# Optimization experiments

Measured on AMD Instinct MI355X. Metric: run time of the kernel, lower is better.

Reference implementation:

```python
import jax, jax.numpy as jnp
import numpy as np

B, N, D = 2, 2048, 1024
H, WS = 16, 128  # num_heads, window_size
DH = D // H
HALF = WS // 2  # window is [i-HALF, i+HALF] inclusive -> 129 keys interior


def setup_inputs() -> dict:
    key = jax.random.key(0)
    ks = jax.random.split(key, 5)
    return {
        "x": jax.random.normal(ks[0], (B, N, D), dtype=jnp.float32),
        "Wqkv": jax.random.normal(ks[1], (D, 3 * D), dtype=jnp.float32) * 0.02,
        "bqkv": jax.random.normal(ks[2], (3 * D,), dtype=jnp.float32) * 0.02,
        "Wout": jax.random.normal(ks[3], (D, D), dtype=jnp.float32) * 0.02,
        "bout": jax.random.normal(ks[4], (D,), dtype=jnp.float32) * 0.02,
    }


def reference(x, Wqkv, bqkv, Wout, bout):
    b, n, d = x.shape
    scale = DH ** -0.5
    qkv = x @ Wqkv + bqkv  # [b, n, 3d]
    q, k, v = jnp.split(qkv, 3, axis=-1)
    # [b, n, d] -> [b, h, n, dh]
    def heads(t):
        return t.reshape(b, n, H, DH).transpose(0, 2, 1, 3)
    q, k, v = heads(q), heads(k), heads(v)
    scores = jnp.einsum("bhid,bhjd->bhij", q, k) * scale  # [b, h, n, n]
    # per-token window [max(0,i-HALF), min(n,i+HALF+1)) == |i-j| <= HALF
    idx = jnp.arange(n)
    band = jnp.abs(idx[:, None] - idx[None, :]) <= HALF  # [n, n]
    neg = jnp.asarray(jnp.finfo(scores.dtype).min, scores.dtype)
    scores = jnp.where(band[None, None], scores, neg)
    attn = jax.nn.softmax(scores, axis=-1)
    out = jnp.einsum("bhij,bhjd->bhid", attn, v)  # [b, h, n, dh]
    out = out.transpose(0, 2, 1, 3).reshape(b, n, d)
    return out @ Wout + bout
```

## Files before the change

### kernel.cpp

```cpp
#include <hip/hip_runtime.h>
#include <hip/hip_bf16.h>
#include <cstdint>
#include <cstddef>

#define BB 2
#define NN 2048
#define DD 1024
#define HH 16
#define DHH 64
#define SCALE 0.125f

typedef _Float16 f16x8 __attribute__((ext_vector_type(8)));
typedef _Float16 f16x4 __attribute__((ext_vector_type(4)));
typedef float f32x4 __attribute__((ext_vector_type(4)));

#define AS1(p) ((__attribute__((address_space(1))) void*)(p))
#define AS3(p) ((__attribute__((address_space(3))) void*)(p))

__global__ __launch_bounds__(256) void prep(const float* __restrict__ x, _Float16* __restrict__ x_h,
                                            const float* __restrict__ Wqkv, _Float16* __restrict__ Wqkv_t,
                                            const float* __restrict__ Wout, _Float16* __restrict__ Wout_t) {
    __shared__ float tile[32][33];
    int bx = blockIdx.x, tid = threadIdx.x;
    if (bx < 2048) {
        int i = bx * 2048 + tid * 8;
        f32x4 a = *(const f32x4*)(x + i);
        f32x4 b = *(const f32x4*)(x + i + 4);
        f16x8 o;
        o[0] = (_Float16)a[0]; o[1] = (_Float16)a[1]; o[2] = (_Float16)a[2]; o[3] = (_Float16)a[3];
        o[4] = (_Float16)b[0]; o[5] = (_Float16)b[1]; o[6] = (_Float16)b[2]; o[7] = (_Float16)b[3];
        *(f16x8*)(x_h + i) = o;
        return;
    }
    const float* in; _Float16* out; int C, tc, tr;
    if (bx < 5120) { int t = bx - 2048; C = 3 * DD; in = Wqkv; out = Wqkv_t; tc = t % 96; tr = t / 96; }
    else           { int t = bx - 5120; C = DD;     in = Wout; out = Wout_t; tc = t % 32; tr = t / 32; }
    int R = DD;
    int txx = tid & 31, ty = tid >> 5;
    int r0 = tr * 32, c0 = tc * 32;
#pragma unroll
    for (int i = 0; i < 32; i += 8)
        tile[ty + i][txx] = in[(size_t)(r0 + ty + i) * C + (c0 + txx)];
    __syncthreads();
#pragma unroll
    for (int i = 0; i < 32; i += 8)
        out[(size_t)(c0 + ty + i) * R + (r0 + txx)] = (_Float16)tile[txx][ty + i];
}

template <bool SWAP, int MT>
__device__ __forceinline__ void gemm_kloop(const _Float16* __restrict__ gA,
                                           const _Float16* __restrict__ gB,
                                           _Float16* lA, _Float16* lB,
                                           const _Float16* As, const _Float16* Bs,
                                           int wm, int wn, int llo, int lhi, int K,
                                           f32x4 acc[][MT > 4 ? MT : 4]) {
    for (int k0 = 0; k0 < K; k0 += 64) {
        __syncthreads();
#pragma unroll
        for (int p = 0; p < MT; ++p)
            __builtin_amdgcn_global_load_lds(AS1(gA + (size_t)p * 8 * K + k0), AS3(lA + p * 512), 16, 0, 0);
#pragma unroll
        for (int p = 0; p < 4; ++p)
            __builtin_amdgcn_global_load_lds(AS1(gB + (size_t)p * 8 * K + k0), AS3(lB + p * 512), 16, 0, 0);
        __syncthreads();

#pragma unroll
        for (int ks = 0; ks < 2; ++ks) {
            f16x8 af[MT], bf[4];
            int swz = (((ks * 4 + lhi) ^ (llo & 7)) * 8);
#pragma unroll
            for (int mt = 0; mt < MT; ++mt)
                af[mt] = *(const f16x8*)(As + (wm + mt * 16 + llo) * 64 + swz);
#pragma unroll
            for (int nt = 0; nt < 4; ++nt)
                bf[nt] = *(const f16x8*)(Bs + (wn + nt * 16 + llo) * 64 + swz);
            if (SWAP) {
#pragma unroll
                for (int nt = 0; nt < 4; ++nt)
#pragma unroll
                    for (int mt = 0; mt < MT; ++mt)
                        acc[nt][mt] = __builtin_amdgcn_mfma_f32_16x16x32_f16(bf[nt], af[mt], acc[nt][mt], 0, 0, 0);
            } else {
#pragma unroll
                for (int mt = 0; mt < MT; ++mt)
#pragma unroll
                    for (int nt = 0; nt < 4; ++nt)
                        acc[mt][nt] = __builtin_amdgcn_mfma_f32_16x16x32_f16(af[mt], bf[nt], acc[mt][nt], 0, 0, 0);
            }
        }
    }
}

__global__ __launch_bounds__(256) void gemm_qkv(const _Float16* __restrict__ A,
                                                const _Float16* __restrict__ Bt,
                                                const float* __restrict__ bias,
                                                _Float16* __restrict__ q_h,
                                                _Float16* __restrict__ k_h,
                                                _Float16* __restrict__ vt_h) {
    const int K = DD;
    __shared__ __align__(16) _Float16 As[128 * 64];
    __shared__ __align__(16) _Float16 Bs[128 * 64];
    int id = blockIdx.x;
    int xcd = id & 7, j = id >> 3;
    int bn = (xcd * 3 + j % 3) * 128;
    int bm = (j / 3) * 128;
    int tid = threadIdx.x;
    int wave = tid >> 6, lane = tid & 63;
    int wm = (wave >> 1) * 64, wn = (wave & 1) * 64;
    int lhi = lane >> 4, llo = lane & 15;

    f32x4 acc[4][4] = {};

    int srow = wave * 32 + (lane >> 3);
    int scol = ((lane & 7) ^ (lane >> 3)) * 8;
    const _Float16* gA = A + (size_t)(bm + srow) * K + scol;
    const _Float16* gB = Bt + (size_t)(bn + srow) * K + scol;
    _Float16* lA = As + wave * 2048 + lane * 8;
    _Float16* lB = Bs + wave * 2048 + lane * 8;

    int region = bn >> 10;
    if (region == 2) {
        gemm_kloop<false, 4>(gA, gB, lA, lB, As, Bs, wm, wn, llo, lhi, K, acc);
#pragma unroll
        for (int nt = 0; nt < 4; ++nt) {
            int col = bn + wn + nt * 16 + llo;
            float bv = bias[col];
            int c = col & 1023;
            int h = c >> 6, dh = c & 63;
#pragma unroll
            for (int mt = 0; mt < 4; ++mt) {
                int row = bm + wm + mt * 16 + lhi * 4;
                int b = row >> 11, n = row & 2047;
                f16x4 v4;
#pragma unroll
                for (int r = 0; r < 4; ++r) v4[r] = (_Float16)(acc[mt][nt][r] + bv);
                *(f16x4*)(vt_h + ((size_t)((b * HH + h) * DHH + dh)) * NN + n) = v4;
            }
        }
    } else {
        gemm_kloop<true, 4>(gA, gB, lA, lB, As, Bs, wm, wn, llo, lhi, K, acc);
        _Float16* dst0 = (region == 0 ? q_h : k_h);
#pragma unroll
        for (int nt = 0; nt < 4; ++nt) {
            int cbase = bn + wn + nt * 16 + lhi * 4;
            f32x4 b4 = *(const f32x4*)(bias + cbase);
            int c = cbase & 1023;
#pragma unroll
            for (int mt = 0; mt < 4; ++mt) {
                int t = bm + wm + mt * 16 + llo;
                int b = t >> 11, n = t & 2047;
                f16x4 v4;
#pragma unroll
                for (int r = 0; r < 4; ++r) v4[r] = (_Float16)(acc[nt][mt][r] + b4[r]);
                *(f16x4*)(dst0 + (size_t)(b * NN + n) * DD + c) = v4;
            }
        }
    }
}

__global__ __launch_bounds__(256) void gemm_out(const _Float16* __restrict__ A,
                                                const _Float16* __restrict__ Bt,
                                                const float* __restrict__ bias,
                                                float* __restrict__ Cf) {
    const int K = DD, N = DD;
    __shared__ __align__(16) _Float16 As[64 * 64];
    __shared__ __align__(16) _Float16 Bs[128 * 64];
    int id = blockIdx.x;
    int xcd = id & 7, j = id >> 3;
    int bm = (xcd * 8 + (j >> 3)) * 64;
    int bn = (j & 7) * 128;
    int tid = threadIdx.x;
    int wave = tid >> 6, lane = tid & 63;
    int wm = (wave >> 1) * 32, wn = (wave & 1) * 64;
    int lhi = lane >> 4, llo = lane & 15;

    f32x4 acc[4][4] = {};

    int srowA = wave * 16 + (lane >> 3);
    int srowB = wave * 32 + (lane >> 3);
    int scol = ((lane & 7) ^ (lane >> 3)) * 8;
    const _Float16* gA = A + (size_t)(bm + srowA) * K + scol;
    const _Float16* gB = Bt + (size_t)(bn + srowB) * K + scol;
    _Float16* lA = As + wave * 1024 + lane * 8;
    _Float16* lB = Bs + wave * 2048 + lane * 8;

    gemm_kloop<true, 2>(gA, gB, lA, lB, As, Bs, wm, wn, llo, lhi, K,
                        (f32x4(*)[4])acc);

#pragma unroll
    for (int nt = 0; nt < 4; ++nt) {
        int cbase = bn + wn + nt * 16 + lhi * 4;
        f32x4 b4 = *(const f32x4*)(bias + cbase);
#pragma unroll
        for (int mt = 0; mt < 2; ++mt) {
            int t = bm + wm + mt * 16 + llo;
            f32x4 v4;
#pragma unroll
            for (int r = 0; r < 4; ++r) v4[r] = acc[nt][mt][r] + b4[r];
            *(f32x4*)(Cf + (size_t)t * N + cbase) = v4;
        }
    }
}

#define KP 64
#define PP 200
#define VP 200
__global__ __launch_bounds__(256) void local_attn(const _Float16* __restrict__ q_h,
                                                  const _Float16* __restrict__ k_h,
                                                  const _Float16* __restrict__ vt_h,
                                                  _Float16* __restrict__ outh) {
    __shared__ __align__(16) _Float16 Ks[192 * KP];
    __shared__ __align__(16) _Float16 Ps[64 * PP];
    __shared__ __align__(16) _Float16 Vt[64 * VP];
    int tid = threadIdx.x;
    int id = blockIdx.x;
    int xcd = id & 7, j = id >> 3;
    int i0 = (xcd * 4 + (j & 3)) * 64;
    int hb = j >> 2;
    int h = hb & 15, b = hb >> 4;

    int wave = tid >> 6, lane = tid & 63;
    int llo = lane & 15, lhi = lane >> 4;

    {
        int srow = lane >> 3;
        int chunk = ((lane & 7) ^ (lane >> 3)) * 8;
        const _Float16* kb = k_h + (size_t)(b * NN) * DD + h * DHH + chunk;
#pragma unroll
        for (int q = 0; q < 6; ++q) {
            int p = wave * 6 + q;
            int jj = i0 - 64 + p * 8 + srow;
            __builtin_amdgcn_global_load_lds(AS1(kb + (ptrdiff_t)jj * DD), AS3(Ks + p * 512 + lane * 8), 16, 0, 0);
        }
    }

    {
        const _Float16* vb = vt_h + (size_t)((b * HH + h) * DHH) * NN + (i0 - 64);
        for (int u = tid; u < 1536; u += 256) {
            int d = u / 24, c = u % 24;
            f16x8 vv = *(const f16x8*)(vb + (ptrdiff_t)d * NN + c * 8);
            *(f16x8*)(Vt + d * VP + c * 8) = vv;
        }
    }

    int qrow = wave * 16 + llo;
    int qi = i0 + qrow;
    const _Float16* qp = q_h + (size_t)(b * NN + qi) * DD + h * DHH;
    f16x8 qf0 = *(const f16x8*)(qp + lhi * 8);
    f16x8 qf1 = *(const f16x8*)(qp + 32 + lhi * 8);
    __syncthreads();

    float sc[12][4];
#pragma unroll
    for (int mt = 0; mt < 12; ++mt) {
        const _Float16* kr = Ks + (mt * 16 + llo) * 64;
        f16x8 kf0 = *(const f16x8*)(kr + ((lhi ^ (llo & 7)) * 8));
        f16x8 kf1 = *(const f16x8*)(kr + (((lhi + 4) ^ (llo & 7)) * 8));
        f32x4 a = {0.f, 0.f, 0.f, 0.f};
        a = __builtin_amdgcn_mfma_f32_16x16x32_f16(kf0, qf0, a, 0, 0, 0);
        a = __builtin_amdgcn_mfma_f32_16x16x32_f16(kf1, qf1, a, 0, 0, 0);
#pragma unroll
        for (int r = 0; r < 4; ++r) sc[mt][r] = a[r];
    }

    float m = -1e30f;
#pragma unroll
    for (int mt = 0; mt < 12; ++mt)
#pragma unroll
        for (int r = 0; r < 4; ++r) {
            int sidx = mt * 16 + lhi * 4 + r;
            int jj = i0 - 64 + sidx;
            int dj = jj - qi;
            bool valid = (jj >= 0) && (jj < NN) && (dj <= 64) && (dj >= -64);
            float v = valid ? sc[mt][r] * SCALE : -1e30f;
            sc[mt][r] = v;
            m = fmaxf(m, v);
        }
    m = fmaxf(m, __shfl_xor(m, 16, 64));
    m = fmaxf(m, __shfl_xor(m, 32, 64));
    float l = 0.f;
#pragma unroll
    for (int mt = 0; mt < 12; ++mt)
#pragma unroll
        for (int r = 0; r < 4; ++r) {
            float e = __expf(sc[mt][r] - m);
            sc[mt][r] = e;
            l += e;
        }
    l += __shfl_xor(l, 16, 64);
    l += __shfl_xor(l, 32, 64);
    float invl = 1.f / l;

#pragma unroll
    for (int mt = 0; mt < 12; ++mt) {
        f16x4 pv;
#pragma unroll
        for (int r = 0; r < 4; ++r) pv[r] = (_Float16)(sc[mt][r] * invl);
        *(f16x4*)(Ps + qrow * PP + mt * 16 + lhi * 4) = pv;
    }
    __asm__ volatile("s_waitcnt lgkmcnt(0)" ::: "memory");

    f32x4 oacc[4] = {};
#pragma unroll
    for (int ks = 0; ks < 6; ++ks) {
        f16x8 pf = *(const f16x8*)(Ps + (wave * 16 + llo) * PP + ks * 32 + lhi * 8);
#pragma unroll
        for (int nt = 0; nt < 4; ++nt) {
            f16x8 vf = *(const f16x8*)(Vt + (nt * 16 + llo) * VP + ks * 32 + lhi * 8);
            oacc[nt] = __builtin_amdgcn_mfma_f32_16x16x32_f16(pf, vf, oacc[nt], 0, 0, 0);
        }
    }

    _Float16* orow = outh + (size_t)(b * NN) * DD + h * DHH;
#pragma unroll
    for (int nt = 0; nt < 4; ++nt)
#pragma unroll
        for (int r = 0; r < 4; ++r) {
            int q = wave * 16 + lhi * 4 + r;
            int d = nt * 16 + llo;
            orow[(size_t)(i0 + q) * DD + d] = (_Float16)oacc[nt][r];
        }
}

extern "C" void kernel_launch(void* const* d_in, const int* in_sizes, int n_in,
                              void* d_out, int out_size, void* d_ws, size_t ws_size,
                              hipStream_t stream) {
    const float* x    = (const float*)d_in[0];
    const float* Wqkv = (const float*)d_in[1];
    const float* bqkv = (const float*)d_in[2];
    const float* Wout = (const float*)d_in[3];
    const float* bout = (const float*)d_in[4];
    float* out = (float*)d_out;

    char* ws = (char*)d_ws;
    _Float16* x_h    = (_Float16*)(ws);
    _Float16* Wqkv_t = (_Float16*)(ws + (size_t)8  * 1024 * 1024);
    _Float16* Wout_t = (_Float16*)(ws + (size_t)14 * 1024 * 1024);
    _Float16* q_h    = (_Float16*)(ws + (size_t)16 * 1024 * 1024);
    _Float16* k_h    = (_Float16*)(ws + (size_t)24 * 1024 * 1024);
    _Float16* vt_h   = (_Float16*)(ws + (size_t)32 * 1024 * 1024);
    _Float16* attn_h = (_Float16*)(ws + (size_t)40 * 1024 * 1024);

    prep<<<6144, 256, 0, stream>>>(x, x_h, Wqkv, Wqkv_t, Wout, Wout_t);

    gemm_qkv<<<768, 256, 0, stream>>>(x_h, Wqkv_t, bqkv, q_h, k_h, vt_h);

    local_attn<<<1024, 256, 0, stream>>>(q_h, k_h, vt_h, attn_h);

    gemm_out<<<512, 256, 0, stream>>>(attn_h, Wout_t, bout, out);
}
```

Measured before the change: 156.8 us.

## Double-buffer LDS tiles in GEMM k-loops to overlap global loads with MFMA

```diff
diff --git a/kernel.cpp b/kernel.cpp
--- a/kernel.cpp
+++ b/kernel.cpp
@@ -48,32 +48,52 @@
 }
 
 template <bool SWAP, int MT>
-__device__ __forceinline__ void gemm_kloop(const _Float16* __restrict__ gA,
-                                           const _Float16* __restrict__ gB,
-                                           _Float16* lA, _Float16* lB,
-                                           const _Float16* As, const _Float16* Bs,
-                                           int wm, int wn, int llo, int lhi, int K,
-                                           f32x4 acc[][MT > 4 ? MT : 4]) {
-    for (int k0 = 0; k0 < K; k0 += 64) {
-        __syncthreads();
-#pragma unroll
-        for (int p = 0; p < MT; ++p)
-            __builtin_amdgcn_global_load_lds(AS1(gA + (size_t)p * 8 * K + k0), AS3(lA + p * 512), 16, 0, 0);
-#pragma unroll
-        for (int p = 0; p < 4; ++p)
-            __builtin_amdgcn_global_load_lds(AS1(gB + (size_t)p * 8 * K + k0), AS3(lB + p * 512), 16, 0, 0);
-        __syncthreads();
-
+__device__ __forceinline__ void gemm_kloop_pipe(const _Float16* __restrict__ gA,
+                                                const _Float16* __restrict__ gB,
+                                                _Float16* lA0, _Float16* lB0,
+                                                _Float16* lA1, _Float16* lB1,
+                                                const _Float16* As0, const _Float16* Bs0,
+                                                const _Float16* As1, const _Float16* Bs1,
+                                                int wm, int wn, int llo, int lhi, int K,
+                                                f32x4 acc[][MT > 4 ? MT : 4]) {
+    const int NIT = K / 64;
+#pragma unroll
+    for (int p = 0; p < MT; ++p)
+        __builtin_amdgcn_global_load_lds(AS1(gA + (size_t)p * 8 * K), AS3(lA0 + p * 512), 16, 0, 0);
+#pragma unroll
+    for (int p = 0; p < 4; ++p)
+        __builtin_amdgcn_global_load_lds(AS1(gB + (size_t)p * 8 * K), AS3(lB0 + p * 512), 16, 0, 0);
+
+    for (int it = 0; it < NIT; ++it) {
+        if (it + 1 < NIT) {
+            int k1 = (it + 1) * 64;
+            _Float16* nlA = (it & 1) ? lA0 : lA1;
+            _Float16* nlB = (it & 1) ? lB0 : lB1;
+#pragma unroll
+            for (int p = 0; p < MT; ++p)
+                __builtin_amdgcn_global_load_lds(AS1(gA + (size_t)p * 8 * K + k1), AS3(nlA + p * 512), 16, 0, 0);
+#pragma unroll
+            for (int p = 0; p < 4; ++p)
+                __builtin_amdgcn_global_load_lds(AS1(gB + (size_t)p * 8 * K + k1), AS3(nlB + p * 512), 16, 0, 0);
+            if (MT == 4) asm volatile("s_waitcnt vmcnt(8)" ::: "memory");
+            else         asm volatile("s_waitcnt vmcnt(6)" ::: "memory");
+        } else {
+            asm volatile("s_waitcnt vmcnt(0)" ::: "memory");
+        }
+        asm volatile("s_barrier" ::: "memory");
+
+        const _Float16* cAs = (it & 1) ? As1 : As0;
+        const _Float16* cBs = (it & 1) ? Bs1 : Bs0;
 #pragma unroll
         for (int ks = 0; ks < 2; ++ks) {
             f16x8 af[MT], bf[4];
             int swz = (((ks * 4 + lhi) ^ (llo & 7)) * 8);
 #pragma unroll
             for (int mt = 0; mt < MT; ++mt)
-                af[mt] = *(const f16x8*)(As + (wm + mt * 16 + llo) * 64 + swz);
+                af[mt] = *(const f16x8*)(cAs + (wm + mt * 16 + llo) * 64 + swz);
 #pragma unroll
             for (int nt = 0; nt < 4; ++nt)
-                bf[nt] = *(const f16x8*)(Bs + (wn + nt * 16 + llo) * 64 + swz);
+                bf[nt] = *(const f16x8*)(cBs + (wn + nt * 16 + llo) * 64 + swz);
             if (SWAP) {
 #pragma unroll
                 for (int nt = 0; nt < 4; ++nt)
@@ -88,6 +108,8 @@
                         acc[mt][nt] = __builtin_amdgcn_mfma_f32_16x16x32_f16(af[mt], bf[nt], acc[mt][nt], 0, 0, 0);
             }
         }
+        asm volatile("s_waitcnt lgkmcnt(0)" ::: "memory");
+        asm volatile("s_barrier" ::: "memory");
     }
 }
 
@@ -98,8 +120,8 @@
                                                 _Float16* __restrict__ k_h,
                                                 _Float16* __restrict__ vt_h) {
     const int K = DD;
-    __shared__ __align__(16) _Float16 As[128 * 64];
-    __shared__ __align__(16) _Float16 Bs[128 * 64];
+    __shared__ __align__(16) _Float16 As0[128 * 64], As1[128 * 64];
+    __shared__ __align__(16) _Float16 Bs0[128 * 64], Bs1[128 * 64];
     int id = blockIdx.x;
     int xcd = id & 7, j = id >> 3;
     int bn = (xcd * 3 + j % 3) * 128;
@@ -115,12 +137,12 @@
     int scol = ((lane & 7) ^ (lane >> 3)) * 8;
     const _Float16* gA = A + (size_t)(bm + srow) * K + scol;
     const _Float16* gB = Bt + (size_t)(bn + srow) * K + scol;
-    _Float16* lA = As + wave * 2048 + lane * 8;
-    _Float16* lB = Bs + wave * 2048 + lane * 8;
+    int loff = wave * 2048 + lane * 8;
 
     int region = bn >> 10;
     if (region == 2) {
-        gemm_kloop<false, 4>(gA, gB, lA, lB, As, Bs, wm, wn, llo, lhi, K, acc);
+        gemm_kloop_pipe<false, 4>(gA, gB, As0 + loff, Bs0 + loff, As1 + loff, Bs1 + loff,
+                                  As0, Bs0, As1, Bs1, wm, wn, llo, lhi, K, acc);
 #pragma unroll
         for (int nt = 0; nt < 4; ++nt) {
             int col = bn + wn + nt * 16 + llo;
@@ -138,7 +160,8 @@
             }
         }
     } else {
-        gemm_kloop<true, 4>(gA, gB, lA, lB, As, Bs, wm, wn, llo, lhi, K, acc);
+        gemm_kloop_pipe<true, 4>(gA, gB, As0 + loff, Bs0 + loff, As1 + loff, Bs1 + loff,
+                                 As0, Bs0, As1, Bs1, wm, wn, llo, lhi, K, acc);
         _Float16* dst0 = (region == 0 ? q_h : k_h);
 #pragma unroll
         for (int nt = 0; nt < 4; ++nt) {
@@ -163,8 +186,8 @@
                                                 const float* __restrict__ bias,
                                                 float* __restrict__ Cf) {
     const int K = DD, N = DD;
-    __shared__ __align__(16) _Float16 As[64 * 64];
-    __shared__ __align__(16) _Float16 Bs[128 * 64];
+    __shared__ __align__(16) _Float16 As0[64 * 64], As1[64 * 64];
+    __shared__ __align__(16) _Float16 Bs0[128 * 64], Bs1[128 * 64];
     int id = blockIdx.x;
     int xcd = id & 7, j = id >> 3;
     int bm = (xcd * 8 + (j >> 3)) * 64;
@@ -181,11 +204,12 @@
     int scol = ((lane & 7) ^ (lane >> 3)) * 8;
     const _Float16* gA = A + (size_t)(bm + srowA) * K + scol;
     const _Float16* gB = Bt + (size_t)(bn + srowB) * K + scol;
-    _Float16* lA = As + wave * 1024 + lane * 8;
-    _Float16* lB = Bs + wave * 2048 + lane * 8;
-
-    gemm_kloop<true, 2>(gA, gB, lA, lB, As, Bs, wm, wn, llo, lhi, K,
-                        (f32x4(*)[4])acc);
+    int loffA = wave * 1024 + lane * 8;
+    int loffB = wave * 2048 + lane * 8;
+
+    gemm_kloop_pipe<true, 2>(gA, gB, As0 + loffA, Bs0 + loffB, As1 + loffA, Bs1 + loffB,
+                             As0, Bs0, As1, Bs1, wm, wn, llo, lhi, K,
+                             (f32x4(*)[4])acc);
 
 #pragma unroll
     for (int nt = 0; nt < 4; ++nt) {
```

Result: slower. 161.2 us (+2.8%).

## Rewrite QKV GEMM to load operands directly into registers, alias attention LDS

Applied to the files above, without the earlier changes.

```diff
diff --git a/kernel.cpp b/kernel.cpp
--- a/kernel.cpp
+++ b/kernel.cpp
@@ -47,6 +47,102 @@
         out[(size_t)(c0 + ty + i) * R + (r0 + txx)] = (_Float16)tile[txx][ty + i];
 }
 
+template <bool SWAP>
+__device__ __forceinline__ void kloop_reg(const _Float16* __restrict__ Abase,
+                                          const _Float16* __restrict__ Bbase,
+                                          int K, f32x4 acc[4][4]) {
+    f16x8 af[2][4], bf[2][4];
+#pragma unroll
+    for (int mt = 0; mt < 4; ++mt) af[0][mt] = *(const f16x8*)(Abase + (size_t)mt * 16 * K);
+#pragma unroll
+    for (int nt = 0; nt < 4; ++nt) bf[0][nt] = *(const f16x8*)(Bbase + (size_t)nt * 16 * K);
+    int cur = 0;
+    for (int ks = 0; ks < K / 32; ++ks) {
+        int nxt = cur ^ 1;
+        if (ks + 1 < K / 32) {
+            int ko = (ks + 1) * 32;
+#pragma unroll
+            for (int mt = 0; mt < 4; ++mt) af[nxt][mt] = *(const f16x8*)(Abase + (size_t)mt * 16 * K + ko);
+#pragma unroll
+            for (int nt = 0; nt < 4; ++nt) bf[nxt][nt] = *(const f16x8*)(Bbase + (size_t)nt * 16 * K + ko);
+        }
+        if (SWAP) {
+#pragma unroll
+            for (int nt = 0; nt < 4; ++nt)
+#pragma unroll
+                for (int mt = 0; mt < 4; ++mt)
+                    acc[nt][mt] = __builtin_amdgcn_mfma_f32_16x16x32_f16(bf[cur][nt], af[cur][mt], acc[nt][mt], 0, 0, 0);
+        } else {
+#pragma unroll
+            for (int mt = 0; mt < 4; ++mt)
+#pragma unroll
+                for (int nt = 0; nt < 4; ++nt)
+                    acc[mt][nt] = __builtin_amdgcn_mfma_f32_16x16x32_f16(af[cur][mt], bf[cur][nt], acc[mt][nt], 0, 0, 0);
+        }
+        cur = nxt;
+    }
+}
+
+__global__ __launch_bounds__(256) void gemm_qkv(const _Float16* __restrict__ A,
+                                                const _Float16* __restrict__ Bt,
+                                                const float* __restrict__ bias,
+                                                _Float16* __restrict__ q_h,
+                                                _Float16* __restrict__ k_h,
+                                                _Float16* __restrict__ vt_h) {
+    const int K = DD;
+    int id = blockIdx.x;
+    int xcd = id & 7, j = id >> 3;
+    int bn = (xcd * 6 + j % 6) * 64;
+    int bm = (j / 6) * 256;
+    int wave = threadIdx.x >> 6, lane = threadIdx.x & 63;
+    int wm = bm + wave * 64;
+    int lhi = lane >> 4, llo = lane & 15;
+
+    const _Float16* Abase = A + (size_t)(wm + llo) * K + lhi * 8;
+    const _Float16* Bbase = Bt + (size_t)(bn + llo) * K + lhi * 8;
+
+    f32x4 acc[4][4] = {};
+    int region = bn >> 10;
+
+    if (region == 2) {
+        kloop_reg<false>(Abase, Bbase, K, acc);
+#pragma unroll
+        for (int nt = 0; nt < 4; ++nt) {
+            int col = bn + nt * 16 + llo;
+            float bv = bias[col];
+            int c = col & 1023;
+            int h = c >> 6, dh = c & 63;
+#pragma unroll
+            for (int mt = 0; mt < 4; ++mt) {
+                int row = wm + mt * 16 + lhi * 4;
+                int b = row >> 11, n = row & 2047;
+                f16x4 v4;
+#pragma unroll
+                for (int r = 0; r < 4; ++r) v4[r] = (_Float16)(acc[mt][nt][r] + bv);
+                *(f16x4*)(vt_h + ((size_t)((b * HH + h) * DHH + dh)) * NN + n) = v4;
+            }
+        }
+    } else {
+        kloop_reg<true>(Abase, Bbase, K, acc);
+        _Float16* dst0 = (region == 0 ? q_h : k_h);
+#pragma unroll
+        for (int nt = 0; nt < 4; ++nt) {
+            int cbase = bn + nt * 16 + lhi * 4;
+            f32x4 b4 = *(const f32x4*)(bias + cbase);
+            int c = cbase & 1023;
+#pragma unroll
+            for (int mt = 0; mt < 4; ++mt) {
+                int t = wm + mt * 16 + llo;
+                int b = t >> 11, n = t & 2047;
+                f16x4 v4;
+#pragma unroll
+                for (int r = 0; r < 4; ++r) v4[r] = (_Float16)(acc[nt][mt][r] + b4[r]);
+                *(f16x4*)(dst0 + (size_t)(b * NN + n) * DD + c) = v4;
+            }
+        }
+    }
+}
+
 template <bool SWAP, int MT>
 __device__ __forceinline__ void gemm_kloop(const _Float16* __restrict__ gA,
                                            const _Float16* __restrict__ gB,
@@ -86,73 +182,6 @@
 #pragma unroll
                     for (int nt = 0; nt < 4; ++nt)
                         acc[mt][nt] = __builtin_amdgcn_mfma_f32_16x16x32_f16(af[mt], bf[nt], acc[mt][nt], 0, 0, 0);
-            }
-        }
-    }
-}
-
-__global__ __launch_bounds__(256) void gemm_qkv(const _Float16* __restrict__ A,
-                                                const _Float16* __restrict__ Bt,
-                                                const float* __restrict__ bias,
-                                                _Float16* __restrict__ q_h,
-                                                _Float16* __restrict__ k_h,
-                                                _Float16* __restrict__ vt_h) {
-    const int K = DD;
-    __shared__ __align__(16) _Float16 As[128 * 64];
-    __shared__ __align__(16) _Float16 Bs[128 * 64];
-    int id = blockIdx.x;
-    int xcd = id & 7, j = id >> 3;
-    int bn = (xcd * 3 + j % 3) * 128;
-    int bm = (j / 3) * 128;
-    int tid = threadIdx.x;
-    int wave = tid >> 6, lane = tid & 63;
-    int wm = (wave >> 1) * 64, wn = (wave & 1) * 64;
-    int lhi = lane >> 4, llo = lane & 15;
-
-    f32x4 acc[4][4] = {};
-
-    int srow = wave * 32 + (lane >> 3);
-    int scol = ((lane & 7) ^ (lane >> 3)) * 8;
-    const _Float16* gA = A + (size_t)(bm + srow) * K + scol;
-    const _Float16* gB = Bt + (size_t)(bn + srow) * K + scol;
-    _Float16* lA = As + wave * 2048 + lane * 8;
-    _Float16* lB = Bs + wave * 2048 + lane * 8;
-
-    int region = bn >> 10;
-    if (region == 2) {
-        gemm_kloop<false, 4>(gA, gB, lA, lB, As, Bs, wm, wn, llo, lhi, K, acc);
-#pragma unroll
-        for (int nt = 0; nt < 4; ++nt) {
-            int col = bn + wn + nt * 16 + llo;
-            float bv = bias[col];
-            int c = col & 1023;
-            int h = c >> 6, dh = c & 63;
-#pragma unroll
-            for (int mt = 0; mt < 4; ++mt) {
-                int row = bm + wm + mt * 16 + lhi * 4;
-                int b = row >> 11, n = row & 2047;
-                f16x4 v4;
-#pragma unroll
-                for (int r = 0; r < 4; ++r) v4[r] = (_Float16)(acc[mt][nt][r] + bv);
-                *(f16x4*)(vt_h + ((size_t)((b * HH + h) * DHH + dh)) * NN + n) = v4;
-            }
-        }
-    } else {
-        gemm_kloop<true, 4>(gA, gB, lA, lB, As, Bs, wm, wn, llo, lhi, K, acc);
-        _Float16* dst0 = (region == 0 ? q_h : k_h);
-#pragma unroll
-        for (int nt = 0; nt < 4; ++nt) {
-            int cbase = bn + wn + nt * 16 + lhi * 4;
-            f32x4 b4 = *(const f32x4*)(bias + cbase);
-            int c = cbase & 1023;
-#pragma unroll
-            for (int mt = 0; mt < 4; ++mt) {
-                int t = bm + wm + mt * 16 + llo;
-                int b = t >> 11, n = t & 2047;
-                f16x4 v4;
-#pragma unroll
-                for (int r = 0; r < 4; ++r) v4[r] = (_Float16)(acc[nt][mt][r] + b4[r]);
-                *(f16x4*)(dst0 + (size_t)(b * NN + n) * DD + c) = v4;
             }
         }
     }
@@ -209,9 +238,10 @@
                                                   const _Float16* __restrict__ k_h,
                                                   const _Float16* __restrict__ vt_h,
                                                   _Float16* __restrict__ outh) {
-    __shared__ __align__(16) _Float16 Ks[192 * KP];
-    __shared__ __align__(16) _Float16 Ps[64 * PP];
+    __shared__ __align__(16) _Float16 KsPs[64 * PP];
     __shared__ __align__(16) _Float16 Vt[64 * VP];
+    _Float16* Ks = KsPs;
+    _Float16* Ps = KsPs;
     int tid = threadIdx.x;
     int id = blockIdx.x;
     int xcd = id & 7, j = id >> 3;
@@ -262,6 +292,7 @@
 #pragma unroll
         for (int r = 0; r < 4; ++r) sc[mt][r] = a[r];
     }
+    __syncthreads();
 
     float m = -1e30f;
 #pragma unroll
```

New measurement: 210.5 us. +34.3%, slower.

## Enlarge QKV GEMM tile to 256x128 with 512 threads; alias K/P LDS in attention

Applied to the files above, without the earlier changes.

```diff
diff --git a/kernel.cpp b/kernel.cpp
--- a/kernel.cpp
+++ b/kernel.cpp
@@ -47,6 +47,110 @@
         out[(size_t)(c0 + ty + i) * R + (r0 + txx)] = (_Float16)tile[txx][ty + i];
 }
 
+__global__ __launch_bounds__(512) void gemm_qkv(const _Float16* __restrict__ A,
+                                                const _Float16* __restrict__ Bt,
+                                                const float* __restrict__ bias,
+                                                _Float16* __restrict__ q_h,
+                                                _Float16* __restrict__ k_h,
+                                                _Float16* __restrict__ vt_h) {
+    const int K = DD;
+    __shared__ __align__(16) _Float16 As[256 * 64];
+    __shared__ __align__(16) _Float16 Bs[128 * 64];
+    int id = blockIdx.x;
+    int xcd = id & 7, j = id >> 3;
+    int bn = (xcd * 3 + j % 3) * 128;
+    int bm = (j / 3) * 256;
+    int tid = threadIdx.x;
+    int wave = tid >> 6, lane = tid & 63;
+    int wm = (wave >> 1) * 64, wn = (wave & 1) * 64;
+    int lhi = lane >> 4, llo = lane & 15;
+
+    f32x4 acc[4][4] = {};
+
+    int srowA = wave * 32 + (lane >> 3);
+    int srowB = wave * 16 + (lane >> 3);
+    int scol = ((lane & 7) ^ (lane >> 3)) * 8;
+    const _Float16* gA = A + (size_t)(bm + srowA) * K + scol;
+    const _Float16* gB = Bt + (size_t)(bn + srowB) * K + scol;
+    _Float16* lA = As + wave * 2048 + lane * 8;
+    _Float16* lB = Bs + wave * 1024 + lane * 8;
+
+    int region = bn >> 10;
+    bool swap = (region != 2);
+
+    for (int k0 = 0; k0 < K; k0 += 64) {
+        __syncthreads();
+#pragma unroll
+        for (int p = 0; p < 4; ++p)
+            __builtin_amdgcn_global_load_lds(AS1(gA + (size_t)p * 8 * K + k0), AS3(lA + p * 512), 16, 0, 0);
+#pragma unroll
+        for (int p = 0; p < 2; ++p)
+            __builtin_amdgcn_global_load_lds(AS1(gB + (size_t)p * 8 * K + k0), AS3(lB + p * 512), 16, 0, 0);
+        __syncthreads();
+
+#pragma unroll
+        for (int ks = 0; ks < 2; ++ks) {
+            f16x8 af[4], bf[4];
+            int swz = (((ks * 4 + lhi) ^ (llo & 7)) * 8);
+#pragma unroll
+            for (int mt = 0; mt < 4; ++mt)
+                af[mt] = *(const f16x8*)(As + (wm + mt * 16 + llo) * 64 + swz);
+#pragma unroll
+            for (int nt = 0; nt < 4; ++nt)
+                bf[nt] = *(const f16x8*)(Bs + (wn + nt * 16 + llo) * 64 + swz);
+            if (swap) {
+#pragma unroll
+                for (int nt = 0; nt < 4; ++nt)
+#pragma unroll
+                    for (int mt = 0; mt < 4; ++mt)
+                        acc[nt][mt] = __builtin_amdgcn_mfma_f32_16x16x32_f16(bf[nt], af[mt], acc[nt][mt], 0, 0, 0);
+            } else {
+#pragma unroll
+                for (int mt = 0; mt < 4; ++mt)
+#pragma unroll
+                    for (int nt = 0; nt < 4; ++nt)
+                        acc[mt][nt] = __builtin_amdgcn_mfma_f32_16x16x32_f16(af[mt], bf[nt], acc[mt][nt], 0, 0, 0);
+            }
+        }
+    }
+
+    if (region == 2) {
+#pragma unroll
+        for (int nt = 0; nt < 4; ++nt) {
+            int col = bn + wn + nt * 16 + llo;
+            float bv = bias[col];
+            int c = col & 1023;
+            int h = c >> 6, dh = c & 63;
+#pragma unroll
+            for (int mt = 0; mt < 4; ++mt) {
+                int row = bm + wm + mt * 16 + lhi * 4;
+                int b = row >> 11, n = row & 2047;
+                f16x4 v4;
+#pragma unroll
+                for (int r = 0; r < 4; ++r) v4[r] = (_Float16)(acc[mt][nt][r] + bv);
+                *(f16x4*)(vt_h + ((size_t)((b * HH + h) * DHH + dh)) * NN + n) = v4;
+            }
+        }
+    } else {
+        _Float16* dst0 = (region == 0 ? q_h : k_h);
+#pragma unroll
+        for (int nt = 0; nt < 4; ++nt) {
+            int cbase = bn + wn + nt * 16 + lhi * 4;
+            f32x4 b4 = *(const f32x4*)(bias + cbase);
+            int c = cbase & 1023;
+#pragma unroll
+            for (int mt = 0; mt < 4; ++mt) {
+                int t = bm + wm + mt * 16 + llo;
+                int b = t >> 11, n = t & 2047;
+                f16x4 v4;
+#pragma unroll
+                for (int r = 0; r < 4; ++r) v4[r] = (_Float16)(acc[nt][mt][r] + b4[r]);
+                *(f16x4*)(dst0 + (size_t)(b * NN + n) * DD + c) = v4;
+            }
+        }
+    }
+}
+
 template <bool SWAP, int MT>
 __device__ __forceinline__ void gemm_kloop(const _Float16* __restrict__ gA,
                                            const _Float16* __restrict__ gB,
@@ -86,73 +190,6 @@
 #pragma unroll
                     for (int nt = 0; nt < 4; ++nt)
                         acc[mt][nt] = __builtin_amdgcn_mfma_f32_16x16x32_f16(af[mt], bf[nt], acc[mt][nt], 0, 0, 0);
-            }
-        }
-    }
-}
-
-__global__ __launch_bounds__(256) void gemm_qkv(const _Float16* __restrict__ A,
-                                                const _Float16* __restrict__ Bt,
-                                                const float* __restrict__ bias,
-                                                _Float16* __restrict__ q_h,
-                                                _Float16* __restrict__ k_h,
-                                                _Float16* __restrict__ vt_h) {
-    const int K = DD;
-    __shared__ __align__(16) _Float16 As[128 * 64];
-    __shared__ __align__(16) _Float16 Bs[128 * 64];
-    int id = blockIdx.x;
-    int xcd = id & 7, j = id >> 3;
-    int bn = (xcd * 3 + j % 3) * 128;
-    int bm = (j / 3) * 128;
-    int tid = threadIdx.x;
-    int wave = tid >> 6, lane = tid & 63;
-    int wm = (wave >> 1) * 64, wn = (wave & 1) * 64;
-    int lhi = lane >> 4, llo = lane & 15;
-
-    f32x4 acc[4][4] = {};
-
-    int srow = wave * 32 + (lane >> 3);
-    int scol = ((lane & 7) ^ (lane >> 3)) * 8;
-    const _Float16* gA = A + (size_t)(bm + srow) * K + scol;
-    const _Float16* gB = Bt + (size_t)(bn + srow) * K + scol;
-    _Float16* lA = As + wave * 2048 + lane * 8;
-    _Float16* lB = Bs + wave * 2048 + lane * 8;
-
-    int region = bn >> 10;
-    if (region == 2) {
-        gemm_kloop<false, 4>(gA, gB, lA, lB, As, Bs, wm, wn, llo, lhi, K, acc);
-#pragma unroll
-        for (int nt = 0; nt < 4; ++nt) {
-            int col = bn + wn + nt * 16 + llo;
-            float bv = bias[col];
-            int c = col & 1023;
-            int h = c >> 6, dh = c & 63;
-#pragma unroll
-            for (int mt = 0; mt < 4; ++mt) {
-                int row = bm + wm + mt * 16 + lhi * 4;
-                int b = row >> 11, n = row & 2047;
-                f16x4 v4;
-#pragma unroll
-                for (int r = 0; r < 4; ++r) v4[r] = (_Float16)(acc[mt][nt][r] + bv);
-                *(f16x4*)(vt_h + ((size_t)((b * HH + h) * DHH + dh)) * NN + n) = v4;
-            }
-        }
-    } else {
-        gemm_kloop<true, 4>(gA, gB, lA, lB, As, Bs, wm, wn, llo, lhi, K, acc);
-        _Float16* dst0 = (region == 0 ? q_h : k_h);
-#pragma unroll
-        for (int nt = 0; nt < 4; ++nt) {
-            int cbase = bn + wn + nt * 16 + lhi * 4;
-            f32x4 b4 = *(const f32x4*)(bias + cbase);
-            int c = cbase & 1023;
-#pragma unroll
-            for (int mt = 0; mt < 4; ++mt) {
-                int t = bm + wm + mt * 16 + llo;
-                int b = t >> 11, n = t & 2047;
-                f16x4 v4;
-#pragma unroll
-                for (int r = 0; r < 4; ++r) v4[r] = (_Float16)(acc[nt][mt][r] + b4[r]);
-                *(f16x4*)(dst0 + (size_t)(b * NN + n) * DD + c) = v4;
             }
         }
     }
@@ -209,9 +246,10 @@
                                                   const _Float16* __restrict__ k_h,
                                                   const _Float16* __restrict__ vt_h,
                                                   _Float16* __restrict__ outh) {
-    __shared__ __align__(16) _Float16 Ks[192 * KP];
-    __shared__ __align__(16) _Float16 Ps[64 * PP];
+    __shared__ __align__(16) _Float16 KsPs[64 * PP];
     __shared__ __align__(16) _Float16 Vt[64 * VP];
+    _Float16* Ks = KsPs;
+    _Float16* Ps = KsPs;
     int tid = threadIdx.x;
     int id = blockIdx.x;
     int xcd = id & 7, j = id >> 3;
@@ -262,6 +300,7 @@
 #pragma unroll
         for (int r = 0; r < 4; ++r) sc[mt][r] = a[r];
     }
+    __syncthreads();
 
     float m = -1e30f;
 #pragma unroll
@@ -343,7 +382,7 @@
 
     prep<<<6144, 256, 0, stream>>>(x, x_h, Wqkv, Wqkv_t, Wout, Wout_t);
 
-    gemm_qkv<<<768, 256, 0, stream>>>(x_h, Wqkv_t, bqkv, q_h, k_h, vt_h);
+    gemm_qkv<<<384, 512, 0, stream>>>(x_h, Wqkv_t, bqkv, q_h, k_h, vt_h);
 
     local_attn<<<1024, 256, 0, stream>>>(q_h, k_h, vt_h, attn_h);
 
```

Result: slower. 169.2 us (+7.9%).
